# Kernel tuning notes

Hardware: AMD Instinct MI355X
Metric: run time of the kernel (lower is better)

## Reference

```python
import jax, jax.numpy as jnp
import numpy as np

HIDDEN = 4096
N_EXPERTS = 128
TOP_K = 8
N_GROUP = 1
TOPK_GROUP = 1
NORM_TOPK_PROB = True
ROUTED_SCALING = 1.0


def setup_inputs() -> dict:
    key = jax.random.key(0)
    k1, k2, k3 = jax.random.split(key, 3)
    hidden_states = jax.random.normal(k1, (4, 4096, HIDDEN), dtype=jnp.float32)
    weight = jax.random.normal(k2, (N_EXPERTS, HIDDEN), dtype=jnp.float32) * 0.02
    e_score_correction_bias = jax.random.normal(k3, (N_EXPERTS,), dtype=jnp.float32) * 0.02
    return {
        "hidden_states": hidden_states,
        "weight": weight,
        "e_score_correction_bias": e_score_correction_bias,
    }


def reference(hidden_states, weight, e_score_correction_bias):
    # flatten tokens: [T, H]
    h = hidden_states.reshape(-1, HIDDEN).astype(jnp.float32)
    # router logits -> sigmoid scores  [T, E]
    logits = jnp.einsum("th,eh->te", h, weight.astype(jnp.float32))
    scores = jax.nn.sigmoid(logits)
    scores_for_choice = scores + e_score_correction_bias[None, :]
    T = scores.shape[0]
    # group scores: sum of top-2 (bias-corrected) scores within each group  [T, G]
    grouped = scores_for_choice.reshape(T, N_GROUP, N_EXPERTS // N_GROUP)
    group_scores = jax.lax.top_k(grouped, 2)[0].sum(axis=-1)
    # select top groups, build expert mask  [T, E]
    group_idx = jax.lax.top_k(group_scores, TOPK_GROUP)[1]          # [T, topk_group]
    group_mask = jnp.zeros((T, N_GROUP), scores.dtype).at[
        jnp.arange(T)[:, None], group_idx].set(1.0)
    score_mask = jnp.repeat(group_mask, N_EXPERTS // N_GROUP, axis=1)
    masked_scores = jnp.where(score_mask > 0, scores_for_choice, 0.0)
    # final top-k experts over masked scores; weights gathered from raw scores
    topk_indices = jax.lax.top_k(masked_scores, TOP_K)[1]           # [T, top_k]
    topk_weights = jnp.take_along_axis(scores, topk_indices, axis=1)
    if NORM_TOPK_PROB:
        denom = topk_weights.sum(axis=-1, keepdims=True) + 1e-20
        topk_weights = topk_weights / denom
    topk_weights = topk_weights * ROUTED_SCALING
    return topk_indices, topk_weights
```

## Files before the change

kernel.cpp:

```cpp
#include <hip/hip_runtime.h>
#include <math.h>

#define HIDDEN 4096
#define NEXP   128
#define TOPK   8
#define BM     32
#define BKC    64
#define NCHUNK (HIDDEN / BKC)
#define SS     132

typedef __attribute__((ext_vector_type(8))) short short8;
typedef __attribute__((ext_vector_type(4))) float f32x4;

__device__ __forceinline__ unsigned pack2(unsigned a, unsigned b) {
  return (a >> 16) | (b & 0xFFFF0000u);
}

struct Split3 { uint4 h, m, l; };
__device__ __forceinline__ Split3 split8(float4 a, float4 b) {
  float x[8] = {a.x, a.y, a.z, a.w, b.x, b.y, b.z, b.w};
  unsigned h[8], m[8], l[8];
#pragma unroll
  for (int j = 0; j < 8; ++j) {
    unsigned u  = __float_as_uint(x[j]);
    unsigned hb = (u + 0x8000u) & 0xFFFF0000u;
    float rh    = x[j] - __uint_as_float(hb);
    unsigned um = __float_as_uint(rh);
    unsigned mb = (um + 0x8000u) & 0xFFFF0000u;
    float rm    = rh - __uint_as_float(mb);
    h[j] = hb; m[j] = mb; l[j] = __float_as_uint(rm);
  }
  Split3 s;
  s.h = make_uint4(pack2(h[0],h[1]), pack2(h[2],h[3]), pack2(h[4],h[5]), pack2(h[6],h[7]));
  s.m = make_uint4(pack2(m[0],m[1]), pack2(m[2],m[3]), pack2(m[4],m[5]), pack2(m[6],m[7]));
  s.l = make_uint4(pack2(l[0],l[1]), pack2(l[2],l[3]), pack2(l[4],l[5]), pack2(l[6],l[7]));
  return s;
}

__global__ __launch_bounds__(256) void pack_w_kernel(
    const float* __restrict__ w, ushort* __restrict__ wp)
{
  const int g    = blockIdx.x * 256 + threadIdx.x;
  const int lane = g & 63;
  const int fid  = g >> 6;
  const int et   = fid >> 7;
  const int kc   = fid & 127;
  const int e    = et * 16 + (lane & 15);
  const int k0   = kc * 32 + (lane >> 4) * 8;
  const float4 x0 = *(const float4*)(w + (size_t)e * HIDDEN + k0);
  const float4 x1 = *(const float4*)(w + (size_t)e * HIDDEN + k0 + 4);
  Split3 s = split8(x0, x1);
  uint4* dst = (uint4*)wp + (size_t)fid * 3 * 64;
  dst[0 * 64 + lane] = s.h;
  dst[1 * 64 + lane] = s.m;
  dst[2 * 64 + lane] = s.l;
}

__global__ __launch_bounds__(512, 4) void router_kernel(
    const float*  __restrict__ h,
    const ushort* __restrict__ wp,
    const float*  __restrict__ bias,
    float* __restrict__ out,
    int T)
{
  __shared__ float Ss[BM * SS];
  const int tid  = threadIdx.x;
  const int row0 = blockIdx.x * BM;

  const int wid  = tid >> 6;
  const int wn   = wid & 3;
  const int wk   = wid >> 2;
  const int lane = tid & 63;
  const int lrow = lane & 15;
  const int lk   = lane >> 4;

  const float* pA0 = h + (size_t)(row0 + lrow) * HIDDEN + wk * 32 + lk * 8;
  const float* pA1 = pA0 + (size_t)16 * HIDDEN;

  const ushort* pB0 = wp + (size_t)((wn * 2 + 0) * 128 + wk) * 1536 + (size_t)lane * 8;
  const ushort* pB1 = wp + (size_t)((wn * 2 + 1) * 128 + wk) * 1536 + (size_t)lane * 8;

  f32x4 acc[2][2];
#pragma unroll
  for (int i = 0; i < 2; ++i)
#pragma unroll
    for (int j = 0; j < 2; ++j) acc[i][j] = (f32x4){0.f, 0.f, 0.f, 0.f};

#pragma unroll 2
  for (int c = 0; c < NCHUNK; ++c) {
    short8 bf[2][3];
    const ushort* b0 = pB0 + (size_t)c * 3072;
    const ushort* b1 = pB1 + (size_t)c * 3072;
#pragma unroll
    for (int s = 0; s < 3; ++s) {
      bf[0][s] = *(const short8*)(b0 + s * 512);
      bf[1][s] = *(const short8*)(b1 + s * 512);
    }
    const float4 a00 = *(const float4*)(pA0 + c * BKC);
    const float4 a01 = *(const float4*)(pA0 + c * BKC + 4);
    const float4 a10 = *(const float4*)(pA1 + c * BKC);
    const float4 a11 = *(const float4*)(pA1 + c * BKC + 4);
    short8 af[2][3];
    {
      Split3 s0 = split8(a00, a01);
      af[0][0] = *(short8*)&s0.h; af[0][1] = *(short8*)&s0.m; af[0][2] = *(short8*)&s0.l;
      Split3 s1 = split8(a10, a11);
      af[1][0] = *(short8*)&s1.h; af[1][1] = *(short8*)&s1.m; af[1][2] = *(short8*)&s1.l;
    }
    __builtin_amdgcn_s_setprio(1);
#pragma unroll
    for (int mi = 0; mi < 2; ++mi)
#pragma unroll
      for (int ni = 0; ni < 2; ++ni) {
        f32x4 cc = acc[mi][ni];
        cc = __builtin_amdgcn_mfma_f32_16x16x32_bf16(af[mi][0], bf[ni][0], cc, 0, 0, 0);
        cc = __builtin_amdgcn_mfma_f32_16x16x32_bf16(af[mi][0], bf[ni][1], cc, 0, 0, 0);
        cc = __builtin_amdgcn_mfma_f32_16x16x32_bf16(af[mi][1], bf[ni][0], cc, 0, 0, 0);
        cc = __builtin_amdgcn_mfma_f32_16x16x32_bf16(af[mi][0], bf[ni][2], cc, 0, 0, 0);
        cc = __builtin_amdgcn_mfma_f32_16x16x32_bf16(af[mi][2], bf[ni][0], cc, 0, 0, 0);
        cc = __builtin_amdgcn_mfma_f32_16x16x32_bf16(af[mi][1], bf[ni][1], cc, 0, 0, 0);
        acc[mi][ni] = cc;
      }
    __builtin_amdgcn_s_setprio(0);
  }

  if (wk == 1) {
#pragma unroll
    for (int mi = 0; mi < 2; ++mi)
#pragma unroll
      for (int ni = 0; ni < 2; ++ni)
#pragma unroll
        for (int j = 0; j < 4; ++j)
          Ss[(mi * 16 + lk * 4 + j) * SS + wn * 32 + ni * 16 + lrow] = acc[mi][ni][j];
  }
  __syncthreads();
  if (wk == 0) {
#pragma unroll
    for (int mi = 0; mi < 2; ++mi)
#pragma unroll
      for (int ni = 0; ni < 2; ++ni)
#pragma unroll
        for (int j = 0; j < 4; ++j) {
          const int ixs = (mi * 16 + lk * 4 + j) * SS + wn * 32 + ni * 16 + lrow;
          Ss[ixs] += acc[mi][ni][j];
        }
  }
  __syncthreads();

  const float bb0 = bias[lane];
  const float bb1 = bias[lane + 64];

  for (int t = wid; t < BM; t += 8) {
    const float lg0 = Ss[t * SS + lane];
    const float lg1 = Ss[t * SS + 64 + lane];
    const float s0 = 1.0f / (1.0f + expf(-lg0));
    const float s1 = 1.0f / (1.0f + expf(-lg1));
    float c0 = s0 + bb0;
    float c1 = s1 + bb1;

    int   sel_i[TOPK];
    float sel_r[TOPK];
    float rsum = 0.0f;
#pragma unroll
    for (int j = 0; j < TOPK; ++j) {
      const bool take0 = (c0 >= c1);
      float v  = take0 ? c0 : c1;
      float rr = take0 ? s0 : s1;
      int   ii = take0 ? lane : lane + 64;
#pragma unroll
      for (int off = 32; off > 0; off >>= 1) {
        const float ov  = __shfl_xor(v, off, 64);
        const float orr = __shfl_xor(rr, off, 64);
        const int   oi  = __shfl_xor(ii, off, 64);
        if (ov > v || (ov == v && oi < ii)) { v = ov; rr = orr; ii = oi; }
      }
      sel_i[j] = ii;
      sel_r[j] = rr;
      rsum += rr;
      if (ii == lane)      c0 = -__builtin_inff();
      if (ii == lane + 64) c1 = -__builtin_inff();
    }
    if (lane == 0) {
      const float inv = 1.0f / (rsum + 1e-20f);
      const size_t tok = (size_t)(row0 + t);
#pragma unroll
      for (int j = 0; j < TOPK; ++j) {
        out[tok * TOPK + j]                    = (float)sel_i[j];
        out[(size_t)T * TOPK + tok * TOPK + j] = sel_r[j] * inv;
      }
    }
  }
}

extern "C" void kernel_launch(void* const* d_in, const int* in_sizes, int n_in,
                              void* d_out, int out_size, void* d_ws, size_t ws_size,
                              hipStream_t stream) {
  const float* h    = (const float*)d_in[0];
  const float* w    = (const float*)d_in[1];
  const float* bias = (const float*)d_in[2];
  float* out = (float*)d_out;
  ushort* wp = (ushort*)d_ws;
  const int T = in_sizes[0] / HIDDEN;

  hipLaunchKernelGGL(pack_w_kernel, dim3(256), dim3(256), 0, stream, w, wp);

  dim3 grid(T / BM);
  dim3 block(512);
  hipLaunchKernelGGL(router_kernel, grid, block, 0, stream, h, wp, bias, out, T);
}
```

Before: 507.8 us.

## Double the row tile and software-pipeline weight and activation loads

Raises the rows per block from 32 to 64, so each wave holds four M-fragments and each weight fragment load is reused across twice as many rows, halving total weight traffic. The K loop becomes a triple-buffered register pipeline: weight fragments are prefetched two chunks ahead and activations one chunk ahead, with a sched_barrier to keep the loads issued early. Register pressure rises, so the launch bounds drop to 2 blocks per CU, and the grid halves, which lowers occupancy and the number of blocks available to fill the GPU.

```diff
diff --git a/kernel.cpp b/kernel.cpp
--- a/kernel.cpp
+++ b/kernel.cpp
@@ -4,7 +4,7 @@
 #define HIDDEN 4096
 #define NEXP   128
 #define TOPK   8
-#define BM     32
+#define BM     64
 #define BKC    64
 #define NCHUNK (HIDDEN / BKC)
 #define SS     132
@@ -56,7 +56,7 @@
   dst[2 * 64 + lane] = s.l;
 }
 
-__global__ __launch_bounds__(512, 4) void router_kernel(
+__global__ __launch_bounds__(512, 2) void router_kernel(
     const float*  __restrict__ h,
     const ushort* __restrict__ wp,
     const float*  __restrict__ bias,
@@ -74,59 +74,86 @@
   const int lrow = lane & 15;
   const int lk   = lane >> 4;
 
-  const float* pA0 = h + (size_t)(row0 + lrow) * HIDDEN + wk * 32 + lk * 8;
-  const float* pA1 = pA0 + (size_t)16 * HIDDEN;
+  const float* pA[4];
+#pragma unroll
+  for (int mi = 0; mi < 4; ++mi)
+    pA[mi] = h + (size_t)(row0 + mi * 16 + lrow) * HIDDEN + wk * 32 + lk * 8;
 
   const ushort* pB0 = wp + (size_t)((wn * 2 + 0) * 128 + wk) * 1536 + (size_t)lane * 8;
   const ushort* pB1 = wp + (size_t)((wn * 2 + 1) * 128 + wk) * 1536 + (size_t)lane * 8;
 
-  f32x4 acc[2][2];
-#pragma unroll
-  for (int i = 0; i < 2; ++i)
+  f32x4 acc[4][2];
+#pragma unroll
+  for (int i = 0; i < 4; ++i)
 #pragma unroll
     for (int j = 0; j < 2; ++j) acc[i][j] = (f32x4){0.f, 0.f, 0.f, 0.f};
 
-#pragma unroll 2
-  for (int c = 0; c < NCHUNK; ++c) {
-    short8 bf[2][3];
-    const ushort* b0 = pB0 + (size_t)c * 3072;
-    const ushort* b1 = pB1 + (size_t)c * 3072;
-#pragma unroll
-    for (int s = 0; s < 3; ++s) {
-      bf[0][s] = *(const short8*)(b0 + s * 512);
-      bf[1][s] = *(const short8*)(b1 + s * 512);
-    }
-    const float4 a00 = *(const float4*)(pA0 + c * BKC);
-    const float4 a01 = *(const float4*)(pA0 + c * BKC + 4);
-    const float4 a10 = *(const float4*)(pA1 + c * BKC);
-    const float4 a11 = *(const float4*)(pA1 + c * BKC + 4);
-    short8 af[2][3];
-    {
-      Split3 s0 = split8(a00, a01);
-      af[0][0] = *(short8*)&s0.h; af[0][1] = *(short8*)&s0.m; af[0][2] = *(short8*)&s0.l;
-      Split3 s1 = split8(a10, a11);
-      af[1][0] = *(short8*)&s1.h; af[1][1] = *(short8*)&s1.m; af[1][2] = *(short8*)&s1.l;
-    }
-    __builtin_amdgcn_s_setprio(1);
-#pragma unroll
-    for (int mi = 0; mi < 2; ++mi)
-#pragma unroll
-      for (int ni = 0; ni < 2; ++ni) {
-        f32x4 cc = acc[mi][ni];
-        cc = __builtin_amdgcn_mfma_f32_16x16x32_bf16(af[mi][0], bf[ni][0], cc, 0, 0, 0);
-        cc = __builtin_amdgcn_mfma_f32_16x16x32_bf16(af[mi][0], bf[ni][1], cc, 0, 0, 0);
-        cc = __builtin_amdgcn_mfma_f32_16x16x32_bf16(af[mi][1], bf[ni][0], cc, 0, 0, 0);
-        cc = __builtin_amdgcn_mfma_f32_16x16x32_bf16(af[mi][0], bf[ni][2], cc, 0, 0, 0);
-        cc = __builtin_amdgcn_mfma_f32_16x16x32_bf16(af[mi][2], bf[ni][0], cc, 0, 0, 0);
-        cc = __builtin_amdgcn_mfma_f32_16x16x32_bf16(af[mi][1], bf[ni][1], cc, 0, 0, 0);
-        acc[mi][ni] = cc;
-      }
-    __builtin_amdgcn_s_setprio(0);
-  }
+  short8 bf0[2][3], bf1[2][3], bf2[2][3];
+  float4 ar[4][2];
+
+#define LOAD_B(slot, cidx)                                                \
+  {                                                                       \
+    const ushort* b0_ = pB0 + (size_t)(cidx) * 3072;                      \
+    const ushort* b1_ = pB1 + (size_t)(cidx) * 3072;                      \
+    _Pragma("unroll")                                                     \
+    for (int s_ = 0; s_ < 3; ++s_) {                                      \
+      slot[0][s_] = *(const short8*)(b0_ + s_ * 512);                     \
+      slot[1][s_] = *(const short8*)(b1_ + s_ * 512);                     \
+    }                                                                     \
+  }
+
+#pragma unroll
+  for (int mi = 0; mi < 4; ++mi) {
+    ar[mi][0] = *(const float4*)(pA[mi]);
+    ar[mi][1] = *(const float4*)(pA[mi] + 4);
+  }
+  LOAD_B(bf0, 0)
+  LOAD_B(bf1, 1)
+
+#define BODY(slot, nslot, c, pref)                                        \
+  {                                                                       \
+    if (pref) { const int cb_ = ((c) + 2 > 63) ? 63 : ((c) + 2);          \
+                LOAD_B(nslot, cb_) }                                      \
+    __builtin_amdgcn_sched_barrier(0);                                    \
+    _Pragma("unroll")                                                     \
+    for (int mi = 0; mi < 4; ++mi) {                                      \
+      Split3 s_ = split8(ar[mi][0], ar[mi][1]);                           \
+      short8 afh = *(short8*)&s_.h;                                       \
+      short8 afm = *(short8*)&s_.m;                                       \
+      short8 afl = *(short8*)&s_.l;                                       \
+      if (pref) {                                                         \
+        ar[mi][0] = *(const float4*)(pA[mi] + ((c) + 1) * BKC);           \
+        ar[mi][1] = *(const float4*)(pA[mi] + ((c) + 1) * BKC + 4);       \
+      }                                                                   \
+      __builtin_amdgcn_s_setprio(1);                                      \
+      _Pragma("unroll")                                                   \
+      for (int ni = 0; ni < 2; ++ni) {                                    \
+        f32x4 cc = acc[mi][ni];                                           \
+        cc = __builtin_amdgcn_mfma_f32_16x16x32_bf16(afh, slot[ni][0], cc, 0, 0, 0); \
+        cc = __builtin_amdgcn_mfma_f32_16x16x32_bf16(afh, slot[ni][1], cc, 0, 0, 0); \
+        cc = __builtin_amdgcn_mfma_f32_16x16x32_bf16(afm, slot[ni][0], cc, 0, 0, 0); \
+        cc = __builtin_amdgcn_mfma_f32_16x16x32_bf16(afh, slot[ni][2], cc, 0, 0, 0); \
+        cc = __builtin_amdgcn_mfma_f32_16x16x32_bf16(afl, slot[ni][0], cc, 0, 0, 0); \
+        cc = __builtin_amdgcn_mfma_f32_16x16x32_bf16(afm, slot[ni][1], cc, 0, 0, 0); \
+        acc[mi][ni] = cc;                                                 \
+      }                                                                   \
+      __builtin_amdgcn_s_setprio(0);                                      \
+    }                                                                     \
+  }
+
+  for (int c3 = 0; c3 < 63; c3 += 3) {
+    BODY(bf0, bf2, c3 + 0, true)
+    BODY(bf1, bf0, c3 + 1, true)
+    BODY(bf2, bf1, c3 + 2, true)
+  }
+  BODY(bf0, bf2, 63, false)
+
+#undef BODY
+#undef LOAD_B
 
   if (wk == 1) {
 #pragma unroll
-    for (int mi = 0; mi < 2; ++mi)
+    for (int mi = 0; mi < 4; ++mi)
 #pragma unroll
       for (int ni = 0; ni < 2; ++ni)
 #pragma unroll
@@ -136,7 +163,7 @@
   __syncthreads();
   if (wk == 0) {
 #pragma unroll
-    for (int mi = 0; mi < 2; ++mi)
+    for (int mi = 0; mi < 4; ++mi)
 #pragma unroll
       for (int ni = 0; ni < 2; ++ni)
 #pragma unroll
```

Result: slower. 522.6 us (+2.9%).

## Stage split activations and weights in double-buffered LDS with async loads

Applied to the files above, without the earlier changes.

Raises the token tile from 32 to 64 rows. Activations are loaded and split into three bf16 parts once per block into swizzled shared memory, and the packed weights are prefetched with global_load_lds into a double buffer, so each chunk's loads overlap the MFMA work of the previous chunk. The aim is to stop every wave from reloading and re-splitting the same A rows and to hide global latency. In exchange it uses more LDS and launch bounds of one block, which lowers occupancy and adds a barrier per chunk.

```diff
diff --git a/kernel.cpp b/kernel.cpp
--- a/kernel.cpp
+++ b/kernel.cpp
@@ -4,10 +4,14 @@
 #define HIDDEN 4096
 #define NEXP   128
 #define TOPK   8
-#define BM     32
+#define BM     64
 #define BKC    64
 #define NCHUNK (HIDDEN / BKC)
 #define SS     132
+
+#define BUFU 36864
+#define BOFF 12288
+#define SMEM_USHORT (2 * BUFU)
 
 typedef __attribute__((ext_vector_type(8))) short short8;
 typedef __attribute__((ext_vector_type(4))) float f32x4;
@@ -56,14 +60,20 @@
   dst[2 * 64 + lane] = s.l;
 }
 
-__global__ __launch_bounds__(512, 4) void router_kernel(
+__device__ __forceinline__ void glds16(const ushort* g, ushort* l) {
+  __builtin_amdgcn_global_load_lds(
+      (const __attribute__((address_space(1))) unsigned int*)g,
+      (__attribute__((address_space(3))) unsigned int*)l, 16, 0, 0);
+}
+
+__global__ __launch_bounds__(512, 1) void router_kernel(
     const float*  __restrict__ h,
     const ushort* __restrict__ wp,
     const float*  __restrict__ bias,
     float* __restrict__ out,
     int T)
 {
-  __shared__ float Ss[BM * SS];
+  __shared__ __align__(16) ushort smem_u[SMEM_USHORT];
   const int tid  = threadIdx.x;
   const int row0 = blockIdx.x * BM;
 
@@ -74,42 +84,93 @@
   const int lrow = lane & 15;
   const int lk   = lane >> 4;
 
-  const float* pA0 = h + (size_t)(row0 + lrow) * HIDDEN + wk * 32 + lk * 8;
-  const float* pA1 = pA0 + (size_t)16 * HIDDEN;
-
-  const ushort* pB0 = wp + (size_t)((wn * 2 + 0) * 128 + wk) * 1536 + (size_t)lane * 8;
-  const ushort* pB1 = wp + (size_t)((wn * 2 + 1) * 128 + wk) * 1536 + (size_t)lane * 8;
-
-  f32x4 acc[2][2];
-#pragma unroll
-  for (int i = 0; i < 2; ++i)
+  const int sr = tid >> 3;
+  const int sk = tid & 7;
+  const float* gA = h + (size_t)(row0 + sr) * HIDDEN + sk * 8;
+  const int six   = (sr * 64 + sk * 8) ^ ((sr & 7) << 3);
+
+  int aix[4];
+#pragma unroll
+  for (int mi = 0; mi < 4; ++mi)
+    aix[mi] = ((mi * 16 + lrow) * 64 + wk * 32 + lk * 8) ^ ((lrow & 7) << 3);
+
+  int bB[2];
+#pragma unroll
+  for (int ni = 0; ni < 2; ++ni)
+    bB[ni] = BOFF + ((wn * 2 + ni) * 2 + wk) * 3 * 512;
+
+#define STAGE_B(ct, bb)                                                     \
+  {                                                                         \
+    _Pragma("unroll")                                                       \
+    for (int ni_ = 0; ni_ < 2; ++ni_) {                                     \
+      const ushort* src_ = wp                                               \
+          + (size_t)((wn * 2 + ni_) * 128 + (ct) * 2 + wk) * 1536           \
+          + (size_t)lane * 8;                                               \
+      ushort* dst_ = smem_u + (bb) + bB[ni_];                               \
+      _Pragma("unroll")                                                     \
+      for (int s_ = 0; s_ < 3; ++s_)                                        \
+        glds16(src_ + s_ * 512, dst_ + s_ * 512);                           \
+    }                                                                       \
+  }
+
+  f32x4 acc[4][2];
+#pragma unroll
+  for (int i = 0; i < 4; ++i)
 #pragma unroll
     for (int j = 0; j < 2; ++j) acc[i][j] = (f32x4){0.f, 0.f, 0.f, 0.f};
 
-#pragma unroll 2
+  float4 pa0 = *(const float4*)(gA);
+  float4 pa1 = *(const float4*)(gA + 4);
+  {
+    Split3 s = split8(pa0, pa1);
+    *(uint4*)(smem_u + 0 * 4096 + six) = s.h;
+    *(uint4*)(smem_u + 1 * 4096 + six) = s.m;
+    *(uint4*)(smem_u + 2 * 4096 + six) = s.l;
+  }
+  pa0 = *(const float4*)(gA + BKC);
+  pa1 = *(const float4*)(gA + BKC + 4);
+  __builtin_amdgcn_sched_barrier(0);
+  STAGE_B(0, 0)
+  __builtin_amdgcn_sched_barrier(0);
+  asm volatile("s_waitcnt lgkmcnt(0)" ::: "memory");
+  __builtin_amdgcn_s_barrier();
+
   for (int c = 0; c < NCHUNK; ++c) {
+    const int cur = (c & 1) * BUFU;
+    const int nxt = ((c + 1) & 1) * BUFU;
+
+    {
+      Split3 s = split8(pa0, pa1);
+      *(uint4*)(smem_u + nxt + 0 * 4096 + six) = s.h;
+      *(uint4*)(smem_u + nxt + 1 * 4096 + six) = s.m;
+      *(uint4*)(smem_u + nxt + 2 * 4096 + six) = s.l;
+    }
+    const int cA = (c + 2 < NCHUNK) ? c + 2 : NCHUNK - 1;
+    pa0 = *(const float4*)(gA + cA * BKC);
+    pa1 = *(const float4*)(gA + cA * BKC + 4);
+    __builtin_amdgcn_sched_barrier(0);
+    const int cB = (c + 1 < NCHUNK) ? c + 1 : NCHUNK - 1;
+    STAGE_B(cB, nxt)
+    __builtin_amdgcn_sched_barrier(0);
+    asm volatile("s_waitcnt vmcnt(8)" ::: "memory");
+
+    short8 af[4][3];
+#pragma unroll
+    for (int mi = 0; mi < 4; ++mi) {
+      af[mi][0] = *(const short8*)(smem_u + cur + 0 * 4096 + aix[mi]);
+      af[mi][1] = *(const short8*)(smem_u + cur + 1 * 4096 + aix[mi]);
+      af[mi][2] = *(const short8*)(smem_u + cur + 2 * 4096 + aix[mi]);
+    }
     short8 bf[2][3];
-    const ushort* b0 = pB0 + (size_t)c * 3072;
-    const ushort* b1 = pB1 + (size_t)c * 3072;
-#pragma unroll
-    for (int s = 0; s < 3; ++s) {
-      bf[0][s] = *(const short8*)(b0 + s * 512);
-      bf[1][s] = *(const short8*)(b1 + s * 512);
-    }
-    const float4 a00 = *(const float4*)(pA0 + c * BKC);
-    const float4 a01 = *(const float4*)(pA0 + c * BKC + 4);
-    const float4 a10 = *(const float4*)(pA1 + c * BKC);
-    const float4 a11 = *(const float4*)(pA1 + c * BKC + 4);
-    short8 af[2][3];
-    {
-      Split3 s0 = split8(a00, a01);
-      af[0][0] = *(short8*)&s0.h; af[0][1] = *(short8*)&s0.m; af[0][2] = *(short8*)&s0.l;
-      Split3 s1 = split8(a10, a11);
-      af[1][0] = *(short8*)&s1.h; af[1][1] = *(short8*)&s1.m; af[1][2] = *(short8*)&s1.l;
-    }
+#pragma unroll
+    for (int ni = 0; ni < 2; ++ni)
+#pragma unroll
+      for (int s = 0; s < 3; ++s)
+        bf[ni][s] = *(const short8*)(smem_u + cur + bB[ni] + s * 512 + lane * 8);
+
     __builtin_amdgcn_s_setprio(1);
 #pragma unroll
-    for (int mi = 0; mi < 2; ++mi)
+    for (int mi = 0; mi < 4; ++mi)
 #pragma unroll
       for (int ni = 0; ni < 2; ++ni) {
         f32x4 cc = acc[mi][ni];
@@ -122,11 +183,19 @@
         acc[mi][ni] = cc;
       }
     __builtin_amdgcn_s_setprio(0);
-  }
-
+
+    asm volatile("s_waitcnt lgkmcnt(0)" ::: "memory");
+    __builtin_amdgcn_s_barrier();
+  }
+#undef STAGE_B
+
+  asm volatile("s_waitcnt vmcnt(0) lgkmcnt(0)" ::: "memory");
+  __builtin_amdgcn_s_barrier();
+
+  float* Ss = (float*)smem_u;
   if (wk == 1) {
 #pragma unroll
-    for (int mi = 0; mi < 2; ++mi)
+    for (int mi = 0; mi < 4; ++mi)
 #pragma unroll
       for (int ni = 0; ni < 2; ++ni)
 #pragma unroll
@@ -136,7 +205,7 @@
   __syncthreads();
   if (wk == 0) {
 #pragma unroll
-    for (int mi = 0; mi < 2; ++mi)
+    for (int mi = 0; mi < 4; ++mi)
 #pragma unroll
       for (int ni = 0; ni < 2; ++ni)
 #pragma unroll
```

Result: faster. 442.6 us (-12.9%).

## Double-buffer global loads with inline asm and enlarge row tile to 64

Applied to the files above, without the earlier changes.

Doubles the token tile per block from 32 to 64 rows so each wave reuses its loaded weight fragments across four row sub-tiles. It also replaces the simple loop with an explicitly double-buffered pipeline that issues raw global_load_dwordx4 via inline asm and waits with manual vmcnt counts, so loads for the next chunk overlap the split and MFMA work of the current one. Occupancy hint drops to one block per CU, register pressure rises, and the grid halves, which reduces parallelism across CUs.

```diff
diff --git a/kernel.cpp b/kernel.cpp
--- a/kernel.cpp
+++ b/kernel.cpp
@@ -4,7 +4,7 @@
 #define HIDDEN 4096
 #define NEXP   128
 #define TOPK   8
-#define BM     32
+#define BM     64
 #define BKC    64
 #define NCHUNK (HIDDEN / BKC)
 #define SS     132
@@ -17,8 +17,8 @@
 }
 
 struct Split3 { uint4 h, m, l; };
-__device__ __forceinline__ Split3 split8(float4 a, float4 b) {
-  float x[8] = {a.x, a.y, a.z, a.w, b.x, b.y, b.z, b.w};
+__device__ __forceinline__ Split3 split8v(f32x4 a, f32x4 b) {
+  float x[8] = {a[0], a[1], a[2], a[3], b[0], b[1], b[2], b[3]};
   unsigned h[8], m[8], l[8];
 #pragma unroll
   for (int j = 0; j < 8; ++j) {
@@ -47,16 +47,20 @@
   const int kc   = fid & 127;
   const int e    = et * 16 + (lane & 15);
   const int k0   = kc * 32 + (lane >> 4) * 8;
-  const float4 x0 = *(const float4*)(w + (size_t)e * HIDDEN + k0);
-  const float4 x1 = *(const float4*)(w + (size_t)e * HIDDEN + k0 + 4);
-  Split3 s = split8(x0, x1);
+  const f32x4 x0 = *(const f32x4*)(w + (size_t)e * HIDDEN + k0);
+  const f32x4 x1 = *(const f32x4*)(w + (size_t)e * HIDDEN + k0 + 4);
+  Split3 s = split8v(x0, x1);
   uint4* dst = (uint4*)wp + (size_t)fid * 3 * 64;
   dst[0 * 64 + lane] = s.h;
   dst[1 * 64 + lane] = s.m;
   dst[2 * 64 + lane] = s.l;
 }
 
-__global__ __launch_bounds__(512, 4) void router_kernel(
+#define GL(dst, base, OFFSTR)                                               \
+  asm volatile("global_load_dwordx4 %0, %1, off offset:" OFFSTR             \
+               : "=&v"(dst) : "v"(base));
+
+__global__ __launch_bounds__(512, 1) void router_kernel(
     const float*  __restrict__ h,
     const ushort* __restrict__ wp,
     const float*  __restrict__ bias,
@@ -74,59 +78,83 @@
   const int lrow = lane & 15;
   const int lk   = lane >> 4;
 
-  const float* pA0 = h + (size_t)(row0 + lrow) * HIDDEN + wk * 32 + lk * 8;
-  const float* pA1 = pA0 + (size_t)16 * HIDDEN;
-
-  const ushort* pB0 = wp + (size_t)((wn * 2 + 0) * 128 + wk) * 1536 + (size_t)lane * 8;
-  const ushort* pB1 = wp + (size_t)((wn * 2 + 1) * 128 + wk) * 1536 + (size_t)lane * 8;
-
-  f32x4 acc[2][2];
-#pragma unroll
-  for (int i = 0; i < 2; ++i)
+  const float bb0 = *(volatile const float*)(bias + lane);
+  const float bb1 = *(volatile const float*)(bias + lane + 64);
+
+  const float* aB0 = h + (size_t)(row0 +  0 + lrow) * HIDDEN + wk * 32 + lk * 8;
+  const float* aB1 = h + (size_t)(row0 + 16 + lrow) * HIDDEN + wk * 32 + lk * 8;
+  const float* aB2 = h + (size_t)(row0 + 32 + lrow) * HIDDEN + wk * 32 + lk * 8;
+  const float* aB3 = h + (size_t)(row0 + 48 + lrow) * HIDDEN + wk * 32 + lk * 8;
+  const ushort* bB0 = wp + (size_t)((wn * 2 + 0) * 128 + wk) * 1536 + (size_t)lane * 8;
+  const ushort* bB1 = wp + (size_t)((wn * 2 + 1) * 128 + wk) * 1536 + (size_t)lane * 8;
+
+  f32x4 acc[4][2];
+#pragma unroll
+  for (int i = 0; i < 4; ++i)
 #pragma unroll
     for (int j = 0; j < 2; ++j) acc[i][j] = (f32x4){0.f, 0.f, 0.f, 0.f};
 
-#pragma unroll 2
-  for (int c = 0; c < NCHUNK; ++c) {
-    short8 bf[2][3];
-    const ushort* b0 = pB0 + (size_t)c * 3072;
-    const ushort* b1 = pB1 + (size_t)c * 3072;
-#pragma unroll
-    for (int s = 0; s < 3; ++s) {
-      bf[0][s] = *(const short8*)(b0 + s * 512);
-      bf[1][s] = *(const short8*)(b1 + s * 512);
-    }
-    const float4 a00 = *(const float4*)(pA0 + c * BKC);
-    const float4 a01 = *(const float4*)(pA0 + c * BKC + 4);
-    const float4 a10 = *(const float4*)(pA1 + c * BKC);
-    const float4 a11 = *(const float4*)(pA1 + c * BKC + 4);
-    short8 af[2][3];
-    {
-      Split3 s0 = split8(a00, a01);
-      af[0][0] = *(short8*)&s0.h; af[0][1] = *(short8*)&s0.m; af[0][2] = *(short8*)&s0.l;
-      Split3 s1 = split8(a10, a11);
-      af[1][0] = *(short8*)&s1.h; af[1][1] = *(short8*)&s1.m; af[1][2] = *(short8*)&s1.l;
-    }
-    __builtin_amdgcn_s_setprio(1);
-#pragma unroll
-    for (int mi = 0; mi < 2; ++mi)
-#pragma unroll
-      for (int ni = 0; ni < 2; ++ni) {
-        f32x4 cc = acc[mi][ni];
-        cc = __builtin_amdgcn_mfma_f32_16x16x32_bf16(af[mi][0], bf[ni][0], cc, 0, 0, 0);
-        cc = __builtin_amdgcn_mfma_f32_16x16x32_bf16(af[mi][0], bf[ni][1], cc, 0, 0, 0);
-        cc = __builtin_amdgcn_mfma_f32_16x16x32_bf16(af[mi][1], bf[ni][0], cc, 0, 0, 0);
-        cc = __builtin_amdgcn_mfma_f32_16x16x32_bf16(af[mi][0], bf[ni][2], cc, 0, 0, 0);
-        cc = __builtin_amdgcn_mfma_f32_16x16x32_bf16(af[mi][2], bf[ni][0], cc, 0, 0, 0);
-        cc = __builtin_amdgcn_mfma_f32_16x16x32_bf16(af[mi][1], bf[ni][1], cc, 0, 0, 0);
-        acc[mi][ni] = cc;
-      }
-    __builtin_amdgcn_s_setprio(0);
-  }
+  f32x4  arA[4][2], arB[4][2];
+  short8 bfA[2][3], bfB[2][3];
+
+#define ISSUE(ar, bf)                                                       \
+  GL(ar[0][0], aB0, "0")  GL(ar[0][1], aB0, "16")                           \
+  GL(ar[1][0], aB1, "0")  GL(ar[1][1], aB1, "16")                           \
+  GL(ar[2][0], aB2, "0")  GL(ar[2][1], aB2, "16")                           \
+  GL(ar[3][0], aB3, "0")  GL(ar[3][1], aB3, "16")                           \
+  GL(bf[0][0], bB0, "0")  GL(bf[0][1], bB0, "1024")  GL(bf[0][2], bB0, "2048") \
+  GL(bf[1][0], bB1, "0")  GL(bf[1][1], bB1, "1024")  GL(bf[1][2], bB1, "2048") \
+  aB0 += BKC; aB1 += BKC; aB2 += BKC; aB3 += BKC; bB0 += 3072; bB1 += 3072;
+
+#define WAITC(NSTR)                                                         \
+  asm volatile("s_waitcnt vmcnt(" NSTR ")" ::: "memory");                   \
+  __builtin_amdgcn_sched_barrier(0);
+
+#define COMPUTE(ar, bf)                                                     \
+  _Pragma("unroll")                                                         \
+  for (int mi = 0; mi < 4; ++mi) {                                          \
+    Split3 s_ = split8v(ar[mi][0], ar[mi][1]);                              \
+    short8 afh = *(short8*)&s_.h;                                           \
+    short8 afm = *(short8*)&s_.m;                                           \
+    short8 afl = *(short8*)&s_.l;                                           \
+    __builtin_amdgcn_s_setprio(1);                                          \
+    _Pragma("unroll")                                                       \
+    for (int ni = 0; ni < 2; ++ni) {                                        \
+      f32x4 cc = acc[mi][ni];                                               \
+      cc = __builtin_amdgcn_mfma_f32_16x16x32_bf16(afh, bf[ni][0], cc, 0, 0, 0); \
+      cc = __builtin_amdgcn_mfma_f32_16x16x32_bf16(afh, bf[ni][1], cc, 0, 0, 0); \
+      cc = __builtin_amdgcn_mfma_f32_16x16x32_bf16(afm, bf[ni][0], cc, 0, 0, 0); \
+      cc = __builtin_amdgcn_mfma_f32_16x16x32_bf16(afh, bf[ni][2], cc, 0, 0, 0); \
+      cc = __builtin_amdgcn_mfma_f32_16x16x32_bf16(afl, bf[ni][0], cc, 0, 0, 0); \
+      cc = __builtin_amdgcn_mfma_f32_16x16x32_bf16(afm, bf[ni][1], cc, 0, 0, 0); \
+      acc[mi][ni] = cc;                                                     \
+    }                                                                       \
+    __builtin_amdgcn_s_setprio(0);                                          \
+  }
+
+  ISSUE(arA, bfA)
+  for (int c = 0; c < NCHUNK - 2; c += 2) {
+    ISSUE(arB, bfB)
+    WAITC("14")
+    COMPUTE(arA, bfA)
+    ISSUE(arA, bfA)
+    WAITC("14")
+    COMPUTE(arB, bfB)
+  }
+  ISSUE(arB, bfB)
+  WAITC("14")
+  COMPUTE(arA, bfA)
+  WAITC("0")
+  COMPUTE(arB, bfB)
+
+#undef COMPUTE
+#undef WAITC
+#undef ISSUE
+#undef GL
 
   if (wk == 1) {
 #pragma unroll
-    for (int mi = 0; mi < 2; ++mi)
+    for (int mi = 0; mi < 4; ++mi)
 #pragma unroll
       for (int ni = 0; ni < 2; ++ni)
 #pragma unroll
@@ -136,7 +164,7 @@
   __syncthreads();
   if (wk == 0) {
 #pragma unroll
-    for (int mi = 0; mi < 2; ++mi)
+    for (int mi = 0; mi < 4; ++mi)
 #pragma unroll
       for (int ni = 0; ni < 2; ++ni)
 #pragma unroll
@@ -146,9 +174,6 @@
         }
   }
   __syncthreads();
-
-  const float bb0 = bias[lane];
-  const float bb1 = bias[lane + 64];
 
   for (int t = wid; t < BM; t += 8) {
     const float lg0 = Ss[t * SS + lane];
```

After: 476.6 us. 6.2% less time.
